# Optimization experiments

Measured on AMD Instinct MI355X. Metric: run time of the kernel, lower is better.

## Reference

```python
import jax, jax.numpy as jnp
import numpy as np

EPS = 1e-5

def sage_conv(x, edge_index, w_l, b_l, w_r):
    # PyG SAGEConv with mean aggregation: lin_l(mean of source-neighbor feats per dst) + lin_r(x)
    n = x.shape[0]
    src, dst = edge_index[0], edge_index[1]
    agg = jax.ops.segment_sum(x[src], dst, num_segments=n)  # [N, d]
    deg = jax.ops.segment_sum(jnp.ones((edge_index.shape[1],), x.dtype), dst, num_segments=n)
    agg = agg / jnp.maximum(deg, 1.0)[:, None]
    return agg @ w_l + b_l + x @ w_r

def batchnorm_eval(x, gamma, beta, mean, var):
    return (x - mean) * (gamma * jax.lax.rsqrt(var + EPS)) + beta

def setup_inputs() -> dict:
    key = jax.random.key(0)
    ks = jax.random.split(key, 12)
    N, E, D, H, O = 10000, 160000, 512, 512, 256
    inp = {
        'x': jax.random.normal(ks[0], (N, D), jnp.float32),
        'edge_index': jax.random.randint(ks[1], (2, E), 0, N, jnp.int32),
        'w_l1': jax.random.normal(ks[2], (D, H), jnp.float32) * (1.0 / np.sqrt(D)),
        'b1': jnp.zeros((H,), jnp.float32),
        'w_r1': jax.random.normal(ks[3], (D, H), jnp.float32) * (1.0 / np.sqrt(D)),
        'bn1_gamma': jnp.ones((H,), jnp.float32),
        'bn1_beta': jnp.zeros((H,), jnp.float32),
        'bn1_mean': jax.random.normal(ks[4], (H,), jnp.float32) * 0.1,
        'bn1_var': jax.random.uniform(ks[5], (H,), jnp.float32, 0.5, 1.5),
        'w_l2': jax.random.normal(ks[6], (H, H), jnp.float32) * (1.0 / np.sqrt(H)),
        'b2': jnp.zeros((H,), jnp.float32),
        'w_r2': jax.random.normal(ks[7], (H, H), jnp.float32) * (1.0 / np.sqrt(H)),
        'bn2_gamma': jnp.ones((H,), jnp.float32),
        'bn2_beta': jnp.zeros((H,), jnp.float32),
        'bn2_mean': jax.random.normal(ks[8], (H,), jnp.float32) * 0.1,
        'bn2_var': jax.random.uniform(ks[9], (H,), jnp.float32, 0.5, 1.5),
        'w_l3': jax.random.normal(ks[10], (H, O), jnp.float32) * (1.0 / np.sqrt(H)),
        'b3': jnp.zeros((O,), jnp.float32),
        'w_r3': jax.random.normal(ks[11], (H, O), jnp.float32) * (1.0 / np.sqrt(H)),
    }
    return inp

def reference(x, edge_index, w_l1, b1, w_r1, bn1_gamma, bn1_beta, bn1_mean, bn1_var,
              w_l2, b2, w_r2, bn2_gamma, bn2_beta, bn2_mean, bn2_var,
              w_l3, b3, w_r3):
    # Layer 1: SAGEConv -> BN (eval) -> ReLU (dropout is identity in eval)
    h = sage_conv(x, edge_index, w_l1, b1, w_r1)
    h = jax.nn.relu(batchnorm_eval(h, bn1_gamma, bn1_beta, bn1_mean, bn1_var))
    # Layer 2
    h = sage_conv(h, edge_index, w_l2, b2, w_r2)
    h = jax.nn.relu(batchnorm_eval(h, bn2_gamma, bn2_beta, bn2_mean, bn2_var))
    # Layer 3 (no BN/ReLU)
    return sage_conv(h, edge_index, w_l3, b3, w_r3)
```

## Files before the change

kernel.cpp:

```cpp
#include <hip/hip_runtime.h>

#define NNODE 10000
#define NEDGE 160000
#define DIM   512
#define OUTD  256

using frag8 = __attribute__((ext_vector_type(8))) short;
using f32x4 = __attribute__((ext_vector_type(4))) float;

__device__ __forceinline__ unsigned short f2bf(float f) {
    union { float f; unsigned u; } v; v.f = f;
    unsigned r = (v.u + 0x7fffu + ((v.u >> 16) & 1u)) >> 16;
    return (unsigned short)r;
}
__device__ __forceinline__ float bf2f(unsigned short s) {
    union { unsigned u; float f; } v; v.u = ((unsigned)s) << 16; return v.f;
}

__global__ void k_count(const int* __restrict__ dst, int E, int* __restrict__ deg) {
    int e = blockIdx.x * 256 + threadIdx.x;
    if (e < E) atomicAdd(&deg[dst[e]], 1);
}

__global__ __launch_bounds__(1024) void k_scan(const int* __restrict__ deg,
                                               int* __restrict__ rs,
                                               int* __restrict__ cur, int n, int total) {
    const int tid = threadIdx.x;
    const int CH = 10;
    const int base = tid * CH;
    int vals[CH];
    int tsum = 0;
#pragma unroll
    for (int j = 0; j < CH; j++) {
        int v = (base + j < n) ? deg[base + j] : 0;
        vals[j] = v; tsum += v;
    }
    const int lane = tid & 63, wid = tid >> 6;
    int x = tsum;
#pragma unroll
    for (int d = 1; d < 64; d <<= 1) {
        int y = __shfl_up(x, d, 64);
        if (lane >= d) x += y;
    }
    __shared__ int wt[16];
    if (lane == 63) wt[wid] = x;
    __syncthreads();
    if (tid == 0) {
        int c = 0;
#pragma unroll
        for (int k = 0; k < 16; k++) { int t = wt[k]; wt[k] = c; c += t; }
    }
    __syncthreads();
    int run = wt[wid] + x - tsum;
#pragma unroll
    for (int j = 0; j < CH; j++) {
        if (base + j < n) { rs[base + j] = run; cur[base + j] = run; }
        run += vals[j];
    }
    if (tid == 0) rs[n] = total;
}

__global__ void k_fill(const int* __restrict__ src, const int* __restrict__ dst,
                       int E, int* __restrict__ cur, int* __restrict__ csr) {
    int e = blockIdx.x * 256 + threadIdx.x;
    if (e < E) {
        int p = atomicAdd(&cur[dst[e]], 1);
        csr[p] = src[e];
    }
}

__global__ void k_cast4(const float* __restrict__ in, unsigned short* __restrict__ out, int n4) {
    int i = blockIdx.x * 256 + threadIdx.x;
    if (i < n4) {
        float4 f = ((const float4*)in)[i];
        ushort4 o;
        o.x = f2bf(f.x); o.y = f2bf(f.y); o.z = f2bf(f.z); o.w = f2bf(f.w);
        ((ushort4*)out)[i] = o;
    }
}

__global__ void k_cast_w_all(const float* __restrict__ wl1, const float* __restrict__ wr1,
                             const float* __restrict__ wl2, const float* __restrict__ wr2,
                             const float* __restrict__ wl3, const float* __restrict__ wr3,
                             unsigned short* __restrict__ bt1, unsigned short* __restrict__ bt2,
                             unsigned short* __restrict__ bt3) {
    int i = blockIdx.x * 256 + threadIdx.x;
    const int S = 1024 * 512;
    const float *wl, *wr; unsigned short* bt; int H; int j;
    if (i < S)           { wl = wl1; wr = wr1; bt = bt1; H = 512; j = i; }
    else if (i < 2 * S)  { wl = wl2; wr = wr2; bt = bt2; H = 512; j = i - S; }
    else                 { wl = wl3; wr = wr3; bt = bt3; H = 256; j = i - 2 * S;
                           if (j >= 512 * 512) return; }
    int n = j >> 9, k = j & 511;
    float v = (n < H) ? wl[k * H + n] : wr[k * H + (n - H)];
    bt[j] = f2bf(v);
}

#define TM 128
#define BKK 64

__global__ __launch_bounds__(256) void k_gemm(const unsigned short* __restrict__ A,
                                              const unsigned short* __restrict__ Bt,
                                              unsigned short* __restrict__ C,
                                              int M, int N, int K) {
    __shared__ __align__(16) short As[TM * BKK];
    __shared__ __align__(16) short Bs[TM * BKK];
    const int tid = threadIdx.x;
    const int m0 = blockIdx.x * TM, n0 = blockIdx.y * TM;
    const int w = tid >> 6, lane = tid & 63;
    const int wm = (w >> 1) * 64, wn = (w & 1) * 64;
    const int fr = lane & 15;
    const int fq = lane >> 4;
    const int sw = fr & 7;

    const int srow = w * 8 + (lane >> 3);
    const int scol = (((lane & 7) ^ (lane >> 3)) * 8);
    const short* pa = (const short*)A + (long)(m0 + srow) * K + scol;
    const short* pb = (const short*)Bt + (long)(n0 + srow) * K + scol;
    short* asDst = As + w * 8 * BKK;
    short* bsDst = Bs + w * 8 * BKK;

    f32x4 acc[4][4];
#pragma unroll
    for (int i = 0; i < 4; i++)
#pragma unroll
        for (int j = 0; j < 4; j++)
#pragma unroll
            for (int r = 0; r < 4; r++) acc[i][j][r] = 0.f;

    for (int k0 = 0; k0 < K; k0 += BKK) {
        __syncthreads();
#pragma unroll
        for (int c = 0; c < 4; c++) {
            __builtin_amdgcn_global_load_lds(
                (const __attribute__((address_space(1))) void*)(pa + (long)c * 32 * K + k0),
                (__attribute__((address_space(3))) void*)(asDst + c * 32 * BKK), 16, 0, 0);
            __builtin_amdgcn_global_load_lds(
                (const __attribute__((address_space(1))) void*)(pb + (long)c * 32 * K + k0),
                (__attribute__((address_space(3))) void*)(bsDst + c * 32 * BKK), 16, 0, 0);
        }
        __syncthreads();
#pragma unroll
        for (int ks = 0; ks < 2; ks++) {
            frag8 af[4], bf[4];
#pragma unroll
            for (int i = 0; i < 4; i++) {
                int R = wm + i * 16 + fr;
                af[i] = *(const frag8*)(As + R * BKK + (((ks * 4 + fq) ^ sw) * 8));
            }
#pragma unroll
            for (int j = 0; j < 4; j++) {
                int R = wn + j * 16 + fr;
                bf[j] = *(const frag8*)(Bs + R * BKK + (((ks * 4 + fq) ^ sw) * 8));
            }
#pragma unroll
            for (int i = 0; i < 4; i++)
#pragma unroll
                for (int j = 0; j < 4; j++)
                    acc[i][j] = __builtin_amdgcn_mfma_f32_16x16x32_bf16(af[i], bf[j], acc[i][j], 0, 0, 0);
        }
    }

#pragma unroll
    for (int i = 0; i < 4; i++) {
        int row_base = m0 + wm + i * 16 + fq * 4;
#pragma unroll
        for (int j = 0; j < 4; j++) {
            int col = n0 + wn + j * 16 + fr;
#pragma unroll
            for (int r = 0; r < 4; r++) {
                int row = row_base + r;
                if (row < M) C[(long)row * N + col] = f2bf(acc[i][j][r]);
            }
        }
    }
}

template <int VEC, int MODE>
__global__ __launch_bounds__(64) void k_agg(const unsigned short* __restrict__ TR, int ncols, int hc,
                                            const int* __restrict__ rs, const int* __restrict__ csr,
                                            const float* __restrict__ bias, const float* __restrict__ gamma,
                                            const float* __restrict__ beta, const float* __restrict__ mean,
                                            const float* __restrict__ var,
                                            unsigned short* __restrict__ hout, float* __restrict__ fout) {
    const int n = blockIdx.x;
    const int lane = threadIdx.x;
    const int c = lane * VEC;
    const int s = rs[n], e = rs[n + 1];
    const int cnt = e - s;
    float acc[VEC];
#pragma unroll
    for (int v = 0; v < VEC; v++) acc[v] = 0.f;

    int myidx = (s + lane < e) ? csr[s + lane] : 0;
#pragma unroll 2
    for (int i = 0; i < cnt; i++) {
        const int ii = i & 63;
        if (i && ii == 0) myidx = (s + i + lane < e) ? csr[s + i + lane] : 0;
        const int src = __shfl(myidx, ii, 64);
        const unsigned* p = (const unsigned*)(TR + (long)src * ncols + c);
        unsigned u[VEC / 2];
        if constexpr (VEC == 8) {
            uint4 q = *(const uint4*)p; u[0] = q.x; u[1] = q.y; u[2] = q.z; u[3] = q.w;
        } else {
            uint2 q = *(const uint2*)p; u[0] = q.x; u[1] = q.y;
        }
#pragma unroll
        for (int v = 0; v < VEC / 2; v++) {
            acc[2 * v]     += bf2f((unsigned short)(u[v] & 0xffffu));
            acc[2 * v + 1] += bf2f((unsigned short)(u[v] >> 16));
        }
    }
    const float invd = 1.f / (float)(cnt > 1 ? cnt : 1);
    const unsigned* rp = (const unsigned*)(TR + (long)n * ncols + hc + c);
    unsigned ur[VEC / 2];
    if constexpr (VEC == 8) {
        uint4 q = *(const uint4*)rp; ur[0] = q.x; ur[1] = q.y; ur[2] = q.z; ur[3] = q.w;
    } else {
        uint2 q = *(const uint2*)rp; ur[0] = q.x; ur[1] = q.y;
    }
#pragma unroll
    for (int v = 0; v < VEC; v++) {
        float rv = bf2f((unsigned short)((v & 1) ? (ur[v / 2] >> 16) : (ur[v / 2] & 0xffffu)));
        float val = acc[v] * invd + rv + bias[c + v];
        if constexpr (MODE == 0) {
            float y = (val - mean[c + v]) * (gamma[c + v] * rsqrtf(var[c + v] + 1e-5f)) + beta[c + v];
            y = fmaxf(y, 0.f);
            hout[(long)n * hc + c + v] = f2bf(y);
        } else {
            fout[(long)n * hc + c + v] = val;
        }
    }
}

extern "C" void kernel_launch(void* const* d_in, const int* in_sizes, int n_in,
                              void* d_out, int out_size, void* d_ws, size_t ws_size,
                              hipStream_t stream) {
    const float* x    = (const float*)d_in[0];
    const int*   ei   = (const int*)d_in[1];
    const float* w_l1 = (const float*)d_in[2];
    const float* b1   = (const float*)d_in[3];
    const float* w_r1 = (const float*)d_in[4];
    const float* g1   = (const float*)d_in[5];
    const float* be1  = (const float*)d_in[6];
    const float* m1   = (const float*)d_in[7];
    const float* v1   = (const float*)d_in[8];
    const float* w_l2 = (const float*)d_in[9];
    const float* b2   = (const float*)d_in[10];
    const float* w_r2 = (const float*)d_in[11];
    const float* g2   = (const float*)d_in[12];
    const float* be2  = (const float*)d_in[13];
    const float* m2   = (const float*)d_in[14];
    const float* v2   = (const float*)d_in[15];
    const float* w_l3 = (const float*)d_in[16];
    const float* b3   = (const float*)d_in[17];
    const float* w_r3 = (const float*)d_in[18];
    float* out = (float*)d_out;

    const int N = NNODE, E = NEDGE;
    const int* src = ei;
    const int* dst = ei + E;

    char* w = (char*)d_ws;
    auto alloc = [&](size_t bytes) { void* p = (void*)w; w += (bytes + 255) & ~(size_t)255; return p; };
    int* deg = (int*)alloc((size_t)N * 4);
    int* rs  = (int*)alloc((size_t)(N + 1) * 4);
    int* cur = (int*)alloc((size_t)N * 4);
    int* csr = (int*)alloc((size_t)E * 4);
    unsigned short* xb  = (unsigned short*)alloc((size_t)N * DIM * 2);
    unsigned short* w1t = (unsigned short*)alloc((size_t)1024 * DIM * 2);
    unsigned short* w2t = (unsigned short*)alloc((size_t)1024 * DIM * 2);
    unsigned short* w3t = (unsigned short*)alloc((size_t)512 * DIM * 2);
    unsigned short* tr  = (unsigned short*)alloc((size_t)N * 1024 * 2);
    unsigned short* h   = (unsigned short*)alloc((size_t)N * DIM * 2);
    (void)alloc(256 * 1024);

    hipMemsetAsync(deg, 0, (size_t)N * 4, stream);
    k_count<<<(E + 255) / 256, 256, 0, stream>>>(dst, E, deg);
    k_scan<<<1, 1024, 0, stream>>>(deg, rs, cur, N, E);
    k_fill<<<(E + 255) / 256, 256, 0, stream>>>(src, dst, E, cur, csr);

    k_cast4<<<(N * DIM / 4 + 255) / 256, 256, 0, stream>>>(x, xb, N * DIM / 4);
    {
        int total = 2 * 1024 * 512 + 512 * 512;
        k_cast_w_all<<<(total + 255) / 256, 256, 0, stream>>>(w_l1, w_r1, w_l2, w_r2, w_l3, w_r3,
                                                              w1t, w2t, w3t);
    }

    dim3 gg((N + TM - 1) / TM, 1024 / TM);
    dim3 g3((N + TM - 1) / TM, 512 / TM);

    k_gemm<<<gg, 256, 0, stream>>>(xb, w1t, tr, N, 1024, 512);
    k_agg<8, 0><<<N, 64, 0, stream>>>(tr, 1024, 512, rs, csr, b1, g1, be1, m1, v1, h, nullptr);
    k_gemm<<<gg, 256, 0, stream>>>(h, w2t, tr, N, 1024, 512);
    k_agg<8, 0><<<N, 64, 0, stream>>>(tr, 1024, 512, rs, csr, b2, g2, be2, m2, v2, h, nullptr);
    k_gemm<<<g3, 256, 0, stream>>>(h, w3t, tr, N, 512, 512);
    k_agg<4, 1><<<N, 64, 0, stream>>>(tr, 512, 256, rs, csr, b3, nullptr, nullptr, nullptr, nullptr, nullptr, out);
}
```

Baseline: 279.0 us.

## Aggregate before GEMM with concatenated K and fold BN into GEMM epilogue

Changes the layer order from transform-then-aggregate to aggregate-then-transform. Each layer first gathers and averages neighbor features at width 512, then runs a single GEMM over K=1024 that concatenates the aggregated and self features against stacked [w_l; w_r] weights. Bias and eval batchnorm are folded into per-column scale and shift applied in the GEMM epilogue. Weight casting is rewritten as a tiled LDS transpose and merged with the x cast into one prep kernel. The gather now reads a 512-wide bf16 row instead of a transformed 1024-wide row, at the cost of doubling GEMM K, shrinking the GEMM N tile to 64, and rounding the aggregate to bf16.

```diff
diff --git a/kernel.cpp b/kernel.cpp
--- a/kernel.cpp
+++ b/kernel.cpp
@@ -2,8 +2,6 @@
 
 #define NNODE 10000
 #define NEDGE 160000
-#define DIM   512
-#define OUTD  256
 
 using frag8 = __attribute__((ext_vector_type(8))) short;
 using f32x4 = __attribute__((ext_vector_type(4))) float;
@@ -69,166 +67,180 @@
     }
 }
 
-__global__ void k_cast4(const float* __restrict__ in, unsigned short* __restrict__ out, int n4) {
-    int i = blockIdx.x * 256 + threadIdx.x;
-    if (i < n4) {
-        float4 f = ((const float4*)in)[i];
+__global__ __launch_bounds__(256) void k_prep(
+    const float* __restrict__ x, unsigned short* __restrict__ xb,
+    const float* __restrict__ wl1, const float* __restrict__ wr1,
+    const float* __restrict__ wl2, const float* __restrict__ wr2,
+    const float* __restrict__ wl3, const float* __restrict__ wr3,
+    unsigned short* __restrict__ bt1, unsigned short* __restrict__ bt2,
+    unsigned short* __restrict__ bt3,
+    const float* __restrict__ b1, const float* __restrict__ g1, const float* __restrict__ be1,
+    const float* __restrict__ m1, const float* __restrict__ v1,
+    const float* __restrict__ b2, const float* __restrict__ g2, const float* __restrict__ be2,
+    const float* __restrict__ m2, const float* __restrict__ v2,
+    const float* __restrict__ b3,
+    float* __restrict__ sc1, float* __restrict__ sh1,
+    float* __restrict__ sc2, float* __restrict__ sh2,
+    float* __restrict__ sc3, float* __restrict__ sh3) {
+    const int b = blockIdx.x, tid = threadIdx.x;
+    if (b < 5000) {
+        int i = b * 256 + tid;
+        float4 f = ((const float4*)x)[i];
         ushort4 o;
         o.x = f2bf(f.x); o.y = f2bf(f.y); o.z = f2bf(f.z); o.w = f2bf(f.w);
-        ((ushort4*)out)[i] = o;
-    }
-}
-
-__global__ void k_cast_w_all(const float* __restrict__ wl1, const float* __restrict__ wr1,
-                             const float* __restrict__ wl2, const float* __restrict__ wr2,
-                             const float* __restrict__ wl3, const float* __restrict__ wr3,
-                             unsigned short* __restrict__ bt1, unsigned short* __restrict__ bt2,
-                             unsigned short* __restrict__ bt3) {
-    int i = blockIdx.x * 256 + threadIdx.x;
-    const int S = 1024 * 512;
-    const float *wl, *wr; unsigned short* bt; int H; int j;
-    if (i < S)           { wl = wl1; wr = wr1; bt = bt1; H = 512; j = i; }
-    else if (i < 2 * S)  { wl = wl2; wr = wr2; bt = bt2; H = 512; j = i - S; }
-    else                 { wl = wl3; wr = wr3; bt = bt3; H = 256; j = i - 2 * S;
-                           if (j >= 512 * 512) return; }
-    int n = j >> 9, k = j & 511;
-    float v = (n < H) ? wl[k * H + n] : wr[k * H + (n - H)];
-    bt[j] = f2bf(v);
-}
-
-#define TM 128
-#define BKK 64
-
-__global__ __launch_bounds__(256) void k_gemm(const unsigned short* __restrict__ A,
+        ((ushort4*)xb)[i] = o;
+        return;
+    }
+    if (b == 6280) {
+        for (int t = tid; t < 512; t += 256) {
+            float s1 = g1[t] * rsqrtf(v1[t] + 1e-5f);
+            sc1[t] = s1; sh1[t] = (b1[t] - m1[t]) * s1 + be1[t];
+            float s2 = g2[t] * rsqrtf(v2[t] + 1e-5f);
+            sc2[t] = s2; sh2[t] = (b2[t] - m2[t]) * s2 + be2[t];
+        }
+        if (tid < 256) { sc3[tid] = 1.0f; sh3[tid] = b3[tid]; }
+        return;
+    }
+    __shared__ float t[32][33];
+    int tj = b - 5000;
+    const float* srcp; unsigned short* dstp; int C, koff, ntilesN;
+    if (tj < 1024) {
+        int job = tj >> 8; int tile = tj & 255; C = 512; ntilesN = 16;
+        srcp = (job == 0) ? wl1 : (job == 1) ? wr1 : (job == 2) ? wl2 : wr2;
+        dstp = (job < 2) ? bt1 : bt2; koff = (job & 1) * 512;
+        tj = tile;
+    } else {
+        int jj = tj - 1024; int job = jj >> 7; int tile = jj & 127; C = 256; ntilesN = 8;
+        srcp = (job == 0) ? wl3 : wr3; dstp = bt3; koff = job * 512;
+        tj = tile;
+    }
+    int k0 = (tj / ntilesN) * 32, c0 = (tj % ntilesN) * 32;
+    int tx = tid & 31, ty = tid >> 5;
+#pragma unroll
+    for (int q = 0; q < 4; q++)
+        t[ty + 8 * q][tx] = srcp[(long)(k0 + ty + 8 * q) * C + c0 + tx];
+    __syncthreads();
+#pragma unroll
+    for (int q = 0; q < 4; q++)
+        dstp[(long)(c0 + ty + 8 * q) * 1024 + koff + k0 + tx] = f2bf(t[tx][ty + 8 * q]);
+}
+
+__global__ __launch_bounds__(64) void k_agg(const unsigned short* __restrict__ S,
+                                            const int* __restrict__ rs, const int* __restrict__ csr,
+                                            unsigned short* __restrict__ outb) {
+    const int n = blockIdx.x;
+    const int c = blockIdx.y * 128 + threadIdx.x * 2;
+    const int s = rs[n], e = rs[n + 1];
+    float a0 = 0.f, a1 = 0.f;
+    int i = s;
+    for (; i + 4 <= e; i += 4) {
+        int r0 = csr[i], r1 = csr[i + 1], r2 = csr[i + 2], r3 = csr[i + 3];
+        unsigned u0 = *(const unsigned*)(S + (long)r0 * 512 + c);
+        unsigned u1 = *(const unsigned*)(S + (long)r1 * 512 + c);
+        unsigned u2 = *(const unsigned*)(S + (long)r2 * 512 + c);
+        unsigned u3 = *(const unsigned*)(S + (long)r3 * 512 + c);
+        a0 += bf2f((unsigned short)(u0 & 0xffffu)); a1 += bf2f((unsigned short)(u0 >> 16));
+        a0 += bf2f((unsigned short)(u1 & 0xffffu)); a1 += bf2f((unsigned short)(u1 >> 16));
+        a0 += bf2f((unsigned short)(u2 & 0xffffu)); a1 += bf2f((unsigned short)(u2 >> 16));
+        a0 += bf2f((unsigned short)(u3 & 0xffffu)); a1 += bf2f((unsigned short)(u3 >> 16));
+    }
+    for (; i < e; i++) {
+        unsigned u = *(const unsigned*)(S + (long)csr[i] * 512 + c);
+        a0 += bf2f((unsigned short)(u & 0xffffu)); a1 += bf2f((unsigned short)(u >> 16));
+    }
+    const int cnt = e - s;
+    const float inv = 1.f / (float)(cnt > 1 ? cnt : 1);
+    unsigned o = (unsigned)f2bf(a0 * inv) | ((unsigned)f2bf(a1 * inv) << 16);
+    *(unsigned*)(outb + (long)n * 512 + c) = o;
+}
+
+template <int MODE, int NOUT>
+__global__ __launch_bounds__(256) void k_gemm(const unsigned short* __restrict__ Agg,
+                                              const unsigned short* __restrict__ Self,
                                               const unsigned short* __restrict__ Bt,
-                                              unsigned short* __restrict__ C,
-                                              int M, int N, int K) {
-    __shared__ __align__(16) short As[TM * BKK];
-    __shared__ __align__(16) short Bs[TM * BKK];
+                                              const float* __restrict__ sc, const float* __restrict__ sh,
+                                              unsigned short* __restrict__ hout, float* __restrict__ fout,
+                                              int M) {
+    __shared__ __align__(16) short As[128 * 64];
+    __shared__ __align__(16) short Bs[64 * 64];
     const int tid = threadIdx.x;
-    const int m0 = blockIdx.x * TM, n0 = blockIdx.y * TM;
+    const int m0 = blockIdx.x * 128, n0 = blockIdx.y * 64;
     const int w = tid >> 6, lane = tid & 63;
-    const int wm = (w >> 1) * 64, wn = (w & 1) * 64;
+    const int wm = (w >> 1) * 64, wn = (w & 1) * 32;
     const int fr = lane & 15;
     const int fq = lane >> 4;
     const int sw = fr & 7;
 
     const int srow = w * 8 + (lane >> 3);
     const int scol = (((lane & 7) ^ (lane >> 3)) * 8);
-    const short* pa = (const short*)A + (long)(m0 + srow) * K + scol;
-    const short* pb = (const short*)Bt + (long)(n0 + srow) * K + scol;
-    short* asDst = As + w * 8 * BKK;
-    short* bsDst = Bs + w * 8 * BKK;
-
-    f32x4 acc[4][4];
+    short* asDst = As + w * 8 * 64;
+    short* bsDst = Bs + w * 8 * 64;
+
+    f32x4 acc[4][2];
 #pragma unroll
     for (int i = 0; i < 4; i++)
 #pragma unroll
-        for (int j = 0; j < 4; j++)
+        for (int j = 0; j < 2; j++)
 #pragma unroll
             for (int r = 0; r < 4; r++) acc[i][j][r] = 0.f;
 
-    for (int k0 = 0; k0 < K; k0 += BKK) {
+    for (int k0 = 0; k0 < 1024; k0 += 64) {
+        const short* abase = (const short*)((k0 < 512) ? Agg : Self);
+        const int kk = k0 & 511;
         __syncthreads();
 #pragma unroll
-        for (int c = 0; c < 4; c++) {
+        for (int cch = 0; cch < 4; cch++)
             __builtin_amdgcn_global_load_lds(
-                (const __attribute__((address_space(1))) void*)(pa + (long)c * 32 * K + k0),
-                (__attribute__((address_space(3))) void*)(asDst + c * 32 * BKK), 16, 0, 0);
+                (const __attribute__((address_space(1))) void*)(abase + (long)(m0 + cch * 32 + srow) * 512 + kk + scol),
+                (__attribute__((address_space(3))) void*)(asDst + cch * 32 * 64), 16, 0, 0);
+#pragma unroll
+        for (int cch = 0; cch < 2; cch++)
             __builtin_amdgcn_global_load_lds(
-                (const __attribute__((address_space(1))) void*)(pb + (long)c * 32 * K + k0),
-                (__attribute__((address_space(3))) void*)(bsDst + c * 32 * BKK), 16, 0, 0);
-        }
+                (const __attribute__((address_space(1))) void*)((const short*)Bt + (long)(n0 + cch * 32 + srow) * 1024 + k0 + scol),
+                (__attribute__((address_space(3))) void*)(bsDst + cch * 32 * 64), 16, 0, 0);
         __syncthreads();
 #pragma unroll
         for (int ks = 0; ks < 2; ks++) {
-            frag8 af[4], bf[4];
-#pragma unroll
-            for (int i = 0; i < 4; i++) {
-                int R = wm + i * 16 + fr;
-                af[i] = *(const frag8*)(As + R * BKK + (((ks * 4 + fq) ^ sw) * 8));
-            }
-#pragma unroll
-            for (int j = 0; j < 4; j++) {
-                int R = wn + j * 16 + fr;
-                bf[j] = *(const frag8*)(Bs + R * BKK + (((ks * 4 + fq) ^ sw) * 8));
-            }
+            frag8 af[4], bf[2];
 #pragma unroll
             for (int i = 0; i < 4; i++)
-#pragma unroll
-                for (int j = 0; j < 4; j++)
+                af[i] = *(const frag8*)(As + (wm + i * 16 + fr) * 64 + (((ks * 4 + fq) ^ sw) * 8));
+#pragma unroll
+            for (int j = 0; j < 2; j++)
+                bf[j] = *(const frag8*)(Bs + (wn + j * 16 + fr) * 64 + (((ks * 4 + fq) ^ sw) * 8));
+#pragma unroll
+            for (int i = 0; i < 4; i++)
+#pragma unroll
+                for (int j = 0; j < 2; j++)
                     acc[i][j] = __builtin_amdgcn_mfma_f32_16x16x32_bf16(af[i], bf[j], acc[i][j], 0, 0, 0);
         }
     }
 
+    float scj[2], shj[2];
+#pragma unroll
+    for (int j = 0; j < 2; j++) {
+        int col = n0 + wn + j * 16 + fr;
+        scj[j] = sc[col]; shj[j] = sh[col];
+    }
 #pragma unroll
     for (int i = 0; i < 4; i++) {
-        int row_base = m0 + wm + i * 16 + fq * 4;
-#pragma unroll
-        for (int j = 0; j < 4; j++) {
+        int rowb = m0 + wm + i * 16 + fq * 4;
+#pragma unroll
+        for (int j = 0; j < 2; j++) {
             int col = n0 + wn + j * 16 + fr;
 #pragma unroll
             for (int r = 0; r < 4; r++) {
-                int row = row_base + r;
-                if (row < M) C[(long)row * N + col] = f2bf(acc[i][j][r]);
+                int row = rowb + r;
+                if (row < M) {
+                    float y = acc[i][j][r] * scj[j] + shj[j];
+                    if constexpr (MODE == 0) {
+                        y = fmaxf(y, 0.f);
+                        hout[(long)row * 512 + col] = f2bf(y);
+                    } else {
+                        fout[(long)row * NOUT + col] = y;
+                    }
+                }
             }
-        }
-    }
-}
-
-template <int VEC, int MODE>
-__global__ __launch_bounds__(64) void k_agg(const unsigned short* __restrict__ TR, int ncols, int hc,
-                                            const int* __restrict__ rs, const int* __restrict__ csr,
-                                            const float* __restrict__ bias, const float* __restrict__ gamma,
-                                            const float* __restrict__ beta, const float* __restrict__ mean,
-                                            const float* __restrict__ var,
-                                            unsigned short* __restrict__ hout, float* __restrict__ fout) {
-    const int n = blockIdx.x;
-    const int lane = threadIdx.x;
-    const int c = lane * VEC;
-    const int s = rs[n], e = rs[n + 1];
-    const int cnt = e - s;
-    float acc[VEC];
-#pragma unroll
-    for (int v = 0; v < VEC; v++) acc[v] = 0.f;
-
-    int myidx = (s + lane < e) ? csr[s + lane] : 0;
-#pragma unroll 2
-    for (int i = 0; i < cnt; i++) {
-        const int ii = i & 63;
-        if (i && ii == 0) myidx = (s + i + lane < e) ? csr[s + i + lane] : 0;
-        const int src = __shfl(myidx, ii, 64);
-        const unsigned* p = (const unsigned*)(TR + (long)src * ncols + c);
-        unsigned u[VEC / 2];
-        if constexpr (VEC == 8) {
-            uint4 q = *(const uint4*)p; u[0] = q.x; u[1] = q.y; u[2] = q.z; u[3] = q.w;
-        } else {
-            uint2 q = *(const uint2*)p; u[0] = q.x; u[1] = q.y;
-        }
-#pragma unroll
-        for (int v = 0; v < VEC / 2; v++) {
-            acc[2 * v]     += bf2f((unsigned short)(u[v] & 0xffffu));
-            acc[2 * v + 1] += bf2f((unsigned short)(u[v] >> 16));
-        }
-    }
-    const float invd = 1.f / (float)(cnt > 1 ? cnt : 1);
-    const unsigned* rp = (const unsigned*)(TR + (long)n * ncols + hc + c);
-    unsigned ur[VEC / 2];
-    if constexpr (VEC == 8) {
-        uint4 q = *(const uint4*)rp; ur[0] = q.x; ur[1] = q.y; ur[2] = q.z; ur[3] = q.w;
-    } else {
-        uint2 q = *(const uint2*)rp; ur[0] = q.x; ur[1] = q.y;
-    }
-#pragma unroll
-    for (int v = 0; v < VEC; v++) {
-        float rv = bf2f((unsigned short)((v & 1) ? (ur[v / 2] >> 16) : (ur[v / 2] & 0xffffu)));
-        float val = acc[v] * invd + rv + bias[c + v];
-        if constexpr (MODE == 0) {
-            float y = (val - mean[c + v]) * (gamma[c + v] * rsqrtf(var[c + v] + 1e-5f)) + beta[c + v];
-            y = fmaxf(y, 0.f);
-            hout[(long)n * hc + c + v] = f2bf(y);
-        } else {
-            fout[(long)n * hc + c + v] = val;
         }
     }
 }
@@ -258,8 +270,8 @@
     float* out = (float*)d_out;
 
     const int N = NNODE, E = NEDGE;
-    const int* src = ei;
-    const int* dst = ei + E;
+    const int* srcI = ei;
+    const int* dstI = ei + E;
 
     char* w = (char*)d_ws;
     auto alloc = [&](size_t bytes) { void* p = (void*)w; w += (bytes + 255) & ~(size_t)255; return p; };
@@ -267,33 +279,35 @@
     int* rs  = (int*)alloc((size_t)(N + 1) * 4);
     int* cur = (int*)alloc((size_t)N * 4);
     int* csr = (int*)alloc((size_t)E * 4);
-    unsigned short* xb  = (unsigned short*)alloc((size_t)N * DIM * 2);
-    unsigned short* w1t = (unsigned short*)alloc((size_t)1024 * DIM * 2);
-    unsigned short* w2t = (unsigned short*)alloc((size_t)1024 * DIM * 2);
-    unsigned short* w3t = (unsigned short*)alloc((size_t)512 * DIM * 2);
-    unsigned short* tr  = (unsigned short*)alloc((size_t)N * 1024 * 2);
-    unsigned short* h   = (unsigned short*)alloc((size_t)N * DIM * 2);
+    unsigned short* xb   = (unsigned short*)alloc((size_t)N * 512 * 2);
+    unsigned short* bt1  = (unsigned short*)alloc((size_t)512 * 1024 * 2);
+    unsigned short* bt2  = (unsigned short*)alloc((size_t)512 * 1024 * 2);
+    unsigned short* bt3  = (unsigned short*)alloc((size_t)256 * 1024 * 2);
+    float* sc1 = (float*)alloc(512 * 4); float* sh1 = (float*)alloc(512 * 4);
+    float* sc2 = (float*)alloc(512 * 4); float* sh2 = (float*)alloc(512 * 4);
+    float* sc3 = (float*)alloc(256 * 4); float* sh3 = (float*)alloc(256 * 4);
+    unsigned short* agg_a = (unsigned short*)alloc((size_t)N * 512 * 2);
+    unsigned short* h1    = (unsigned short*)alloc((size_t)N * 512 * 2);
+    unsigned short* h2    = (unsigned short*)alloc((size_t)N * 512 * 2);
     (void)alloc(256 * 1024);
 
     hipMemsetAsync(deg, 0, (size_t)N * 4, stream);
-    k_count<<<(E + 255) / 256, 256, 0, stream>>>(dst, E, deg);
+    k_count<<<(E + 255) / 256, 256, 0, stream>>>(dstI, E, deg);
     k_scan<<<1, 1024, 0, stream>>>(deg, rs, cur, N, E);
-    k_fill<<<(E + 255) / 256, 256, 0, stream>>>(src, dst, E, cur, csr);
-
-    k_cast4<<<(N * DIM / 4 + 255) / 256, 256, 0, stream>>>(x, xb, N * DIM / 4);
-    {
-        int total = 2 * 1024 * 512 + 512 * 512;
-        k_cast_w_all<<<(total + 255) / 256, 256, 0, stream>>>(w_l1, w_r1, w_l2, w_r2, w_l3, w_r3,
-                                                              w1t, w2t, w3t);
-    }
-
-    dim3 gg((N + TM - 1) / TM, 1024 / TM);
-    dim3 g3((N + TM - 1) / TM, 512 / TM);
-
-    k_gemm<<<gg, 256, 0, stream>>>(xb, w1t, tr, N, 1024, 512);
-    k_agg<8, 0><<<N, 64, 0, stream>>>(tr, 1024, 512, rs, csr, b1, g1, be1, m1, v1, h, nullptr);
-    k_gemm<<<gg, 256, 0, stream>>>(h, w2t, tr, N, 1024, 512);
-    k_agg<8, 0><<<N, 64, 0, stream>>>(tr, 1024, 512, rs, csr, b2, g2, be2, m2, v2, h, nullptr);
-    k_gemm<<<g3, 256, 0, stream>>>(h, w3t, tr, N, 512, 512);
-    k_agg<4, 1><<<N, 64, 0, stream>>>(tr, 512, 256, rs, csr, b3, nullptr, nullptr, nullptr, nullptr, nullptr, out);
-}
+    k_fill<<<(E + 255) / 256, 256, 0, stream>>>(srcI, dstI, E, cur, csr);
+    k_prep<<<6281, 256, 0, stream>>>(x, xb, w_l1, w_r1, w_l2, w_r2, w_l3, w_r3,
+                                     bt1, bt2, bt3,
+                                     b1, g1, be1, m1, v1, b2, g2, be2, m2, v2, b3,
+                                     sc1, sh1, sc2, sh2, sc3, sh3);
+
+    dim3 g12((N + 127) / 128, 8);
+    dim3 g3((N + 127) / 128, 4);
+    dim3 ga(N, 4);
+
+    k_agg<<<ga, 64, 0, stream>>>(xb, rs, csr, agg_a);
+    k_gemm<0, 512><<<g12, 256, 0, stream>>>(agg_a, xb, bt1, sc1, sh1, h1, nullptr, N);
+    k_agg<<<ga, 64, 0, stream>>>(h1, rs, csr, agg_a);
+    k_gemm<0, 512><<<g12, 256, 0, stream>>>(agg_a, h1, bt2, sc2, sh2, h2, nullptr, N);
+    k_agg<<<ga, 64, 0, stream>>>(h2, rs, csr, agg_a);
+    k_gemm<1, 256><<<g3, 256, 0, stream>>>(agg_a, h2, bt3, sc3, sh3, nullptr, out, N);
+}
```

New measurement: 275.9 us. No clear change (-1.1%).
